# Performance work log

Measured on AMD Instinct MI355X. Metric: run time of the kernel, lower is better.

The kernel has to match this reference:

```python
import jax, jax.numpy as jnp
from jax import lax
import numpy as np

EPS = 1e-5


def _fps(xyz, S):
    B, N, _ = xyz.shape

    def step(carry, _):
        dist, far = carry  # [B,N], [B]
        c = xyz[jnp.arange(B), far]               # [B,3]
        d = jnp.sum((xyz - c[:, None, :]) ** 2, -1)  # [B,N]
        dist = jnp.minimum(dist, d)
        nxt = jnp.argmax(dist, -1).astype(jnp.int32)
        return (dist, nxt), far

    init = (jnp.full((B, N), 1e10, xyz.dtype), jnp.zeros((B,), jnp.int32))
    _, idxs = lax.scan(step, init, None, length=S)
    return jnp.transpose(idxs)  # [B,S]


def _gather(pts, idx):
    # pts: [B,N,C], idx: [B,...] -> [B,...,C]
    return jax.vmap(lambda p, i: p[i])(pts, idx)


def _conv(x, W, b):
    # 1x1 Conv1d: x [M,Cin,L], W [Cout,Cin], b [Cout]
    return jnp.einsum('mcl,oc->mol', x, W) + b[None, :, None]


def _bn(x, g, b):
    # BatchNorm1d (training-mode batch stats, biased variance)
    mu = jnp.mean(x, (0, 2), keepdims=True)
    v = jnp.var(x, (0, 2), keepdims=True)
    return g[None, :, None] * (x - mu) / jnp.sqrt(v + EPS) + b[None, :, None]


def _forward(xyz, feature, affine_alpha, affine_beta, w_tr, b_tr, g_tr, be_tr,
             w1, b1, g1, be1, w2, b2, groups, k):
    xyz = jnp.transpose(xyz, (0, 2, 1))        # [B,N,3]
    feature = jnp.transpose(feature, (0, 2, 1))  # [B,N,D]
    B, N, _ = xyz.shape
    S = groups
    xyz_ng = lax.stop_gradient(xyz)  # cluster() runs under torch.no_grad
    fps_idx = _fps(xyz_ng, S)                        # [B,S]
    new_xyz = _gather(xyz_ng, fps_idx)               # [B,S,3] (detached)
    # squared-distance kNN: [B,S,N]
    sqr = (jnp.sum(new_xyz ** 2, -1)[:, :, None]
           + jnp.sum(xyz_ng ** 2, -1)[:, None, :]
           - 2.0 * jnp.einsum('bsc,bnc->bsn', new_xyz, xyz_ng))
    _, idx = lax.top_k(-sqr, k)                      # [B,S,k] smallest distances
    new_feature = _gather(feature, fps_idx)          # [B,S,D]
    grouped_xyz = _gather(xyz, idx)                  # [B,S,k,3]
    grouped_feature = _gather(feature, idx)          # [B,S,k,D]
    grouped_feature = jnp.concatenate([grouped_feature, grouped_xyz], -1)  # [B,S,k,D+3]
    # anchor normalization
    mean = jnp.concatenate([new_feature, new_xyz], -1)[:, :, None, :]  # [B,S,1,D+3]
    diff = grouped_feature - mean
    std = jnp.std(diff.reshape(B, -1), axis=-1, ddof=1)[:, None, None, None]
    gf = affine_alpha * (diff / (std + EPS)) + affine_beta
    # concat anchor feature -> [B,S,k,2D+3]
    D = new_feature.shape[-1]
    x = jnp.concatenate([gf, jnp.broadcast_to(new_feature[:, :, None, :], (B, S, k, D))], -1)
    d = x.shape[-1]
    # PreExtraction: [B,S,k,d] -> [B*S,d,k]
    x = jnp.transpose(x, (0, 1, 3, 2)).reshape(B * S, d, k)
    x = jax.nn.relu(_bn(_conv(x, w_tr, b_tr), g_tr, be_tr))
    y = jax.nn.relu(_bn(_conv(x, w1, b1), g1, be1))
    y = _conv(y, w2, b2)
    x = jax.nn.relu(y + x)
    x = jnp.max(x, -1).reshape(B, S, -1)             # adaptive_max_pool1d(1)
    return (jnp.transpose(new_xyz, (0, 2, 1)), jnp.transpose(x, (0, 2, 1)))


def setup_inputs() -> dict:
    key = jax.random.key(0)
    k0, k1, k2, k3, k4 = jax.random.split(key, 5)
    B, N, D = 8, 4096, 64
    return {
        'xyz': jax.random.normal(k0, (B, 3, N), jnp.float32),
        'feature': jax.random.normal(k1, (B, D, N), jnp.float32),
        'affine_alpha': jnp.ones((1, 1, 1, D + 3), jnp.float32),
        'affine_beta': jnp.zeros((1, 1, 1, D + 3), jnp.float32),
        'w_tr': 0.05 * jax.random.normal(k2, (D, 3 + 2 * D), jnp.float32),
        'b_tr': jnp.zeros((D,), jnp.float32),
        'g_tr': jnp.ones((D,), jnp.float32),
        'be_tr': jnp.zeros((D,), jnp.float32),
        'w1': 0.05 * jax.random.normal(k3, (D, D), jnp.float32),
        'b1': jnp.zeros((D,), jnp.float32),
        'g1': jnp.ones((D,), jnp.float32),
        'be1': jnp.zeros((D,), jnp.float32),
        'w2': 0.05 * jax.random.normal(k4, (D, D), jnp.float32),
        'b2': jnp.zeros((D,), jnp.float32),
        'groups': 1024,
        'k': 32,
    }


def reference(xyz, feature, affine_alpha, affine_beta, w_tr, b_tr, g_tr, be_tr,
              w1, b1, g1, be1, w2, b2, groups, k):
    return _forward(xyz, feature, affine_alpha, affine_beta, w_tr, b_tr, g_tr, be_tr,
                    w1, b1, g1, be1, w2, b2, groups, k)
```

## Files before the change

### kernel.cpp

```cpp
#include <hip/hip_runtime.h>
#include <cfloat>
#include <math.h>

#define B_ 8
#define N_ 4096
#define D_ 64
#define S_ 1024
#define K_ 32
#define CIN_ 131

typedef float f32x2 __attribute__((ext_vector_type(2)));

template <int CTRL>
__device__ __forceinline__ unsigned long long dpp_u64(unsigned long long k) {
  int lo = (int)(unsigned int)k, hi = (int)(unsigned int)(k >> 32);
  lo = __builtin_amdgcn_update_dpp(lo, lo, CTRL, 0xf, 0xf, false);
  hi = __builtin_amdgcn_update_dpp(hi, hi, CTRL, 0xf, 0xf, false);
  return ((unsigned long long)(unsigned int)hi << 32) | (unsigned int)lo;
}

__device__ __forceinline__ float wave_max_f32_dpp(float v) {
  int x = __float_as_int(v);
#define STEP(ctrl)                                                        \
  {                                                                       \
    int t = __builtin_amdgcn_update_dpp(x, x, ctrl, 0xf, 0xf, false);     \
    v = fmaxf(v, __int_as_float(t));                                      \
    x = __float_as_int(v);                                                \
  }
  STEP(0x111)
  STEP(0x112)
  STEP(0x114)
  STEP(0x118)
  STEP(0x142)
  STEP(0x143)
#undef STEP
  return __int_as_float(__builtin_amdgcn_readlane(x, 63));
}

__global__ __launch_bounds__(256) void fps_kernel(const float* __restrict__ xyz,
                                                  int* __restrict__ fps_idx,
                                                  float* __restrict__ nxyz,
                                                  float* __restrict__ out0,
                                                  const float* __restrict__ feature,
                                                  float* __restrict__ featT) {
#pragma clang fp contract(off)
  const int tid = threadIdx.x;
  __shared__ __align__(16) float4 sp[N_];
  __shared__ int si[S_];
  __shared__ unsigned long long keyp[2][4];
  if (blockIdx.x >= 8) {
    const int blk = blockIdx.x - 8;
    const int b = blk >> 6, n0 = (blk & 63) * 64;
    float* tile = (float*)sp;
#pragma unroll
    for (int i = 0; i < 16; i++) {
      int c = i * 4 + (tid >> 6), nl = tid & 63;
      tile[c * 65 + nl] = feature[((size_t)b * 64 + c) * N_ + n0 + nl];
    }
    __syncthreads();
#pragma unroll
    for (int i = 0; i < 16; i++) {
      int nl = i * 4 + (tid >> 6), c = tid & 63;
      featT[((size_t)b * N_ + n0 + nl) * 64 + c] = tile[c * 65 + nl];
    }
    return;
  }
  const int b = blockIdx.x;
  const float* xb = xyz + (size_t)b * 3 * N_;
  const float4* xv = (const float4*)xb;
  f32x2 pxv[8], pyv[8], pzv[8];
  float dist[16];
#pragma unroll
  for (int q = 0; q < 4; q++) {
    float4 X = xv[4 * tid + q];
    float4 Y = xv[1024 + 4 * tid + q];
    float4 Z = xv[2048 + 4 * tid + q];
    pxv[2 * q] = (f32x2){X.x, X.y};  pxv[2 * q + 1] = (f32x2){X.z, X.w};
    pyv[2 * q] = (f32x2){Y.x, Y.y};  pyv[2 * q + 1] = (f32x2){Y.z, Y.w};
    pzv[2 * q] = (f32x2){Z.x, Z.y};  pzv[2 * q + 1] = (f32x2){Z.z, Z.w};
  }
#pragma unroll
  for (int j = 0; j < 8; j++) {
    dist[2 * j] = 1e10f;
    dist[2 * j + 1] = 1e10f;
    sp[16 * tid + 2 * j] = make_float4(pxv[j].x, pyv[j].x, pzv[j].x, 0.f);
    sp[16 * tid + 2 * j + 1] = make_float4(pxv[j].y, pyv[j].y, pzv[j].y, 0.f);
  }
  if (tid == 0) si[0] = 0;
  __syncthreads();
  float cx = sp[0].x, cy = sp[0].y, cz = sp[0].z;
  const int wav = tid >> 6, lane = tid & 63;
  for (int s = 1; s < S_; s++) {
    const f32x2 c2x = {cx, cx}, c2y = {cy, cy}, c2z = {cz, cz};
#pragma unroll
    for (int j = 0; j < 8; j++) {
      f32x2 dx = pxv[j] - c2x;
      f32x2 dy = pyv[j] - c2y;
      f32x2 dz = pzv[j] - c2z;
      f32x2 d = (dx * dx + dy * dy) + dz * dz;
      dist[2 * j] = fminf(dist[2 * j], d.x);
      dist[2 * j + 1] = fminf(dist[2 * j + 1], d.y);
    }
    float t8[8], t4[4];
#pragma unroll
    for (int j = 0; j < 8; j++) t8[j] = fmaxf(dist[2 * j], dist[2 * j + 1]);
#pragma unroll
    for (int j = 0; j < 4; j++) t4[j] = fmaxf(t8[2 * j], t8[2 * j + 1]);
    float best = fmaxf(fmaxf(t4[0], t4[1]), fmaxf(t4[2], t4[3]));
    int bi = 16 * tid;
#pragma unroll
    for (int i = 15; i >= 0; i--)
      if (dist[i] == best) bi = 16 * tid + i;
    float wmax = wave_max_f32_dpp(best);
    unsigned long long m = __ballot(best == wmax);
    int l = __ffsll(m) - 1;
    int widx = __builtin_amdgcn_readlane(bi, l);
    if (lane == 0)
      keyp[s & 1][wav] =
          ((unsigned long long)(unsigned int)__float_as_int(wmax) << 32) |
          (unsigned int)(4095 - widx);
    __syncthreads();
    unsigned long long k = keyp[s & 1][lane & 3];
    unsigned long long t;
    t = dpp_u64<0xB1>(k); if (t > k) k = t;
    t = dpp_u64<0x4E>(k); if (t > k) k = t;
    int bix = 4095 - (int)(k & 0xfffull);
    if (tid == 0) si[s] = bix;
    float4 c = sp[bix];
    cx = c.x; cy = c.y; cz = c.z;
  }
  __syncthreads();
  for (int e = tid; e < S_; e += 256) {
    int n = si[e];
    fps_idx[b * S_ + e] = n;
    float4 c = sp[n];
    nxyz[(size_t)(b * S_ + e) * 3 + 0] = c.x;
    nxyz[(size_t)(b * S_ + e) * 3 + 1] = c.y;
    nxyz[(size_t)(b * S_ + e) * 3 + 2] = c.z;
    out0[(size_t)b * 3 * S_ + e] = c.x;
    out0[(size_t)b * 3 * S_ + S_ + e] = c.y;
    out0[(size_t)b * 3 * S_ + 2 * S_ + e] = c.z;
  }
}

__global__ __launch_bounds__(256) void knn_kernel(const float* __restrict__ xyz,
                                                  const float* __restrict__ nxyz,
                                                  int* __restrict__ knn,
                                                  const float* __restrict__ featT,
                                                  const int* __restrict__ fps_i,
                                                  float* __restrict__ nfeat) {
#pragma clang fp contract(off)
  const int bs = blockIdx.x, tid = threadIdx.x;
  if (bs >= 8192) {
    int e = (bs - 8192) * 256 + tid;
    int bsx = e >> 6, c = e & 63;
    int bq = bsx >> 10;
    int n = fps_i[bsx];
    nfeat[e] = featT[((size_t)bq * N_ + n) * 64 + c];
    return;
  }
  const int b = bs >> 10;
  const float* xb = xyz + (size_t)b * 3 * N_;
  const float cx = nxyz[(size_t)bs * 3], cy = nxyz[(size_t)bs * 3 + 1], cz = nxyz[(size_t)bs * 3 + 2];
  const float cn = (cx * cx + cy * cy) + cz * cz;
  const f32x2 c2x = {cx, cx}, c2y = {cy, cy}, c2z = {cz, cz};
  const f32x2 c2n = {cn, cn}, two = {2.0f, 2.0f};
  float d[16];
#pragma unroll
  for (int j = 0; j < 8; j++) {
    int n0 = (2 * j) * 256 + tid, n1 = n0 + 256;
    f32x2 px = {xb[n0], xb[n1]};
    f32x2 py = {xb[N_ + n0], xb[N_ + n1]};
    f32x2 pz = {xb[2 * N_ + n0], xb[2 * N_ + n1]};
    f32x2 pn = (px * px + py * py) + pz * pz;
    f32x2 dot = (c2x * px + c2y * py) + c2z * pz;
    f32x2 dd = (c2n + pn) - two * dot;
    d[2 * j] = dd.x;
    d[2 * j + 1] = dd.y;
  }
  float mv = FLT_MAX;
  int mi = tid;
#pragma unroll
  for (int i = 0; i < 16; i++)
    if (d[i] < mv) { mv = d[i]; mi = i * 256 + tid; }
  __shared__ unsigned long long keyp[2][4];
  __shared__ int skk[K_];
  const int wav = tid >> 6, lane = tid & 63;
  for (int j = 0; j < K_; j++) {
    unsigned int u = __float_as_uint(mv);
    u ^= ((unsigned int)((int)u >> 31) | 0x80000000u);
    unsigned long long key = ((unsigned long long)u << 32) | (unsigned int)mi;
#pragma unroll
    for (int off = 32; off >= 1; off >>= 1) {
      unsigned long long ok = __shfl_xor(key, off);
      if (ok < key) key = ok;
    }
    if (lane == 0) keyp[j & 1][wav] = key;
    __syncthreads();
    unsigned long long kmin = keyp[j & 1][0];
#pragma unroll
    for (int w = 1; w < 4; w++) {
      unsigned long long k2 = keyp[j & 1][w];
      if (k2 < kmin) kmin = k2;
    }
    int g = (int)(kmin & 0xffffffffull);
    if (tid == 0) skk[j] = g;
    if ((g & 255) == tid) {
      int sl = g >> 8;
#pragma unroll
      for (int i = 0; i < 16; i++)
        if (i == sl) d[i] = FLT_MAX;
      mv = FLT_MAX; mi = tid;
#pragma unroll
      for (int i = 0; i < 16; i++)
        if (d[i] < mv) { mv = d[i]; mi = i * 256 + tid; }
    }
  }
  __syncthreads();
  if (tid < K_) knn[(size_t)bs * K_ + tid] = skk[tid];
}

__global__ __launch_bounds__(256) void gather_nf(const float* __restrict__ feature,
                                                 const int* __restrict__ fps_i,
                                                 float* __restrict__ nfeat) {
  int e = blockIdx.x * 256 + threadIdx.x;
  int b = e >> 16, rem = e & 65535;
  int s = rem >> 6, c = rem & 63;
  int n = fps_i[b * S_ + s];
  nfeat[e] = feature[((size_t)b * 64 + c) * N_ + n];
}

__global__ __launch_bounds__(256) void std_partial(const float* __restrict__ feature,
                                                   const float* __restrict__ xyz,
                                                   const float* __restrict__ nxyz,
                                                   const float* __restrict__ nfeat,
                                                   const int* __restrict__ knn,
                                                   float* __restrict__ outp) {
  const int blk = blockIdx.x, tid = threadIdx.x;
  const int b = blk >> 6, chunk = blk & 63;
  float s = 0.f, q = 0.f;
  for (int e = tid; e < 16 * K_ * 67; e += 256) {
    int so = e / (K_ * 67);
    int rem = e - so * (K_ * 67);
    int kk = rem / 67;
    int c = rem - kk * 67;
    int bs = b * S_ + chunk * 16 + so;
    int n = knn[(size_t)bs * K_ + kk];
    float raw = (c < 64) ? feature[((size_t)b * 64 + c) * N_ + n]
                         : xyz[((size_t)b * 3 + (c - 64)) * N_ + n];
    float anc = (c < 64) ? nfeat[(size_t)bs * 64 + c]
                         : nxyz[(size_t)bs * 3 + (c - 64)];
    float dd = raw - anc;
    s += dd; q += dd * dd;
  }
#pragma unroll
  for (int off = 32; off >= 1; off >>= 1) { s += __shfl_xor(s, off); q += __shfl_xor(q, off); }
  __shared__ float rs[4], rq[4];
  if ((tid & 63) == 0) { rs[tid >> 6] = s; rq[tid >> 6] = q; }
  __syncthreads();
  if (tid == 0) {
    outp[blk * 2] = rs[0] + rs[1] + rs[2] + rs[3];
    outp[blk * 2 + 1] = rq[0] + rq[1] + rq[2] + rq[3];
  }
}

__global__ void std_final(const float* __restrict__ part, float* __restrict__ invstd) {
  int b = threadIdx.x;
  if (b < B_) {
    double s = 0.0, q = 0.0;
    for (int i = 0; i < 64; i++) {
      s += (double)part[(b * 64 + i) * 2];
      q += (double)part[(b * 64 + i) * 2 + 1];
    }
    const double n = (double)(S_ * K_ * 67);
    double var = (q - s * s / n) / (n - 1.0);
    invstd[b] = (float)(1.0 / (sqrt(var) + 1e-5));
  }
}

template <int MODE>
__global__ __launch_bounds__(256, 2) void mlp_kernel(
    const float* __restrict__ feature, const float* __restrict__ xyz,
    const float* __restrict__ nxyz, const float* __restrict__ nfeat,
    const int* __restrict__ knn, const float* __restrict__ invstd,
    const float* __restrict__ alpha, const float* __restrict__ beta,
    const float* __restrict__ w_tr, const float* __restrict__ b_tr,
    const float* __restrict__ w1, const float* __restrict__ b1,
    const float* __restrict__ w2, const float* __restrict__ b2,
    const float* __restrict__ bn_tr, const float* __restrict__ bn_1,
    float* __restrict__ bnpart, float* __restrict__ out1) {
  __shared__ __align__(16) float pool[15556];
  float* Wt = pool;
  float* xin = pool + 8516;
  float* ub = xin;
  float* tb = pool + 8516 + 4192;
  float* part = pool + 8516 + 4192 + 2304;
  int* sknn = (int*)(part + 512);
  const int bs = blockIdx.x, tid = threadIdx.x;
  const int b = bs >> 10, s = bs & 1023;
  if (tid < K_) sknn[tid] = knn[(size_t)bs * K_ + tid];
  for (int e = tid; e < 64 * 131; e += 256) {
    int o = e / 131, c = e - o * 131;
    Wt[c * 65 + o] = w_tr[e];
  }
  __syncthreads();
  const float inv = invstd[b];
  for (int e = tid; e < CIN_ * K_; e += 256) {
    int c = e >> 5, kk = e & 31;
    float v;
    if (c < 67) {
      int n = sknn[kk];
      float raw = (c < 64) ? feature[((size_t)b * 64 + c) * N_ + n]
                           : xyz[((size_t)b * 3 + (c - 64)) * N_ + n];
      float anc = (c < 64) ? nfeat[(size_t)bs * 64 + c]
                           : nxyz[(size_t)bs * 3 + (c - 64)];
      v = alpha[c] * ((raw - anc) * inv) + beta[c];
    } else {
      v = nfeat[(size_t)bs * 64 + (c - 67)];
    }
    xin[e] = v;
  }
  __syncthreads();
  const int o = tid & 63, kkb = (tid >> 6) * 8;
  float acc[8];
  {
    float bv = b_tr[o];
#pragma unroll
    for (int j = 0; j < 8; j++) acc[j] = bv;
  }
  for (int c = 0; c < CIN_; c++) {
    float w = Wt[c * 65 + o];
    const float4 xa = *(const float4*)(xin + c * 32 + kkb);
    const float4 xb4 = *(const float4*)(xin + c * 32 + kkb + 4);
    acc[0] += w * xa.x; acc[1] += w * xa.y; acc[2] += w * xa.z; acc[3] += w * xa.w;
    acc[4] += w * xb4.x; acc[5] += w * xb4.y; acc[6] += w * xb4.z; acc[7] += w * xb4.w;
  }
  if (MODE == 0) {
    float s8 = 0.f, q8 = 0.f;
#pragma unroll
    for (int j = 0; j < 8; j++) { s8 += acc[j]; q8 += acc[j] * acc[j]; }
    part[(tid >> 6) * 64 + o] = s8;
    part[256 + (tid >> 6) * 64 + o] = q8;
    __syncthreads();
    if (tid < 64) {
      float ss = 0.f, qq = 0.f;
      for (int g = 0; g < 4; g++) { ss += part[g * 64 + tid]; qq += part[256 + g * 64 + tid]; }
      bnpart[(size_t)bs * 128 + tid] = ss;
      bnpart[(size_t)bs * 128 + 64 + tid] = qq;
    }
    return;
  }
  float tv[8];
  {
    float sc = bn_tr[o], sh = bn_tr[64 + o];
#pragma unroll
    for (int j = 0; j < 8; j++) {
      tv[j] = fmaxf(fmaf(sc, acc[j], sh), 0.f);
      tb[o * 36 + kkb + j] = tv[j];
    }
  }
  __syncthreads();
  for (int e = tid; e < 64 * 64; e += 256) {
    int oo = e >> 6, c = e & 63;
    Wt[c * 65 + oo] = w1[e];
  }
  __syncthreads();
  float acc2[8];
  {
    float bv = b1[o];
#pragma unroll
    for (int j = 0; j < 8; j++) acc2[j] = bv;
  }
  for (int c = 0; c < 64; c++) {
    float w = Wt[c * 65 + o];
    const float4 ta = *(const float4*)(tb + c * 36 + kkb);
    const float4 ta2 = *(const float4*)(tb + c * 36 + kkb + 4);
    acc2[0] += w * ta.x; acc2[1] += w * ta.y; acc2[2] += w * ta.z; acc2[3] += w * ta.w;
    acc2[4] += w * ta2.x; acc2[5] += w * ta2.y; acc2[6] += w * ta2.z; acc2[7] += w * ta2.w;
  }
  if (MODE == 1) {
    float s8 = 0.f, q8 = 0.f;
#pragma unroll
    for (int j = 0; j < 8; j++) { s8 += acc2[j]; q8 += acc2[j] * acc2[j]; }
    part[(tid >> 6) * 64 + o] = s8;
    part[256 + (tid >> 6) * 64 + o] = q8;
    __syncthreads();
    if (tid < 64) {
      float ss = 0.f, qq = 0.f;
      for (int g = 0; g < 4; g++) { ss += part[g * 64 + tid]; qq += part[256 + g * 64 + tid]; }
      bnpart[(size_t)bs * 128 + tid] = ss;
      bnpart[(size_t)bs * 128 + 64 + tid] = qq;
    }
    return;
  }
  {
    float sc = bn_1[o], sh = bn_1[64 + o];
#pragma unroll
    for (int j = 0; j < 8; j++) ub[o * 36 + kkb + j] = fmaxf(fmaf(sc, acc2[j], sh), 0.f);
  }
  __syncthreads();
  for (int e = tid; e < 64 * 64; e += 256) {
    int oo = e >> 6, c = e & 63;
    Wt[c * 65 + oo] = w2[e];
  }
  __syncthreads();
  float acc3[8];
  {
    float bv = b2[o];
#pragma unroll
    for (int j = 0; j < 8; j++) acc3[j] = bv;
  }
  for (int c = 0; c < 64; c++) {
    float w = Wt[c * 65 + o];
    const float4 ua = *(const float4*)(ub + c * 36 + kkb);
    const float4 ua2 = *(const float4*)(ub + c * 36 + kkb + 4);
    acc3[0] += w * ua.x; acc3[1] += w * ua.y; acc3[2] += w * ua.z; acc3[3] += w * ua.w;
    acc3[4] += w * ua2.x; acc3[5] += w * ua2.y; acc3[6] += w * ua2.z; acc3[7] += w * ua2.w;
  }
  float m = 0.f;
#pragma unroll
  for (int j = 0; j < 8; j++) m = fmaxf(m, fmaxf(acc3[j] + tv[j], 0.f));
  part[(tid >> 6) * 64 + o] = m;
  __syncthreads();
  if (tid < 64) {
    float mm = part[tid];
    for (int g = 1; g < 4; g++) mm = fmaxf(mm, part[g * 64 + tid]);
    out1[((size_t)b * 64 + tid) * S_ + s] = mm;
  }
}

__global__ __launch_bounds__(256) void bn_finalize(const float* __restrict__ part,
                                                   const float* __restrict__ g,
                                                   const float* __restrict__ be,
                                                   float* __restrict__ bnout) {
  const int ch = blockIdx.x, tid = threadIdx.x;
  double s = 0.0, q = 0.0;
  for (int i = tid; i < B_ * S_; i += 256) {
    s += (double)part[(size_t)i * 128 + ch];
    q += (double)part[(size_t)i * 128 + 64 + ch];
  }
#pragma unroll
  for (int off = 32; off >= 1; off >>= 1) { s += __shfl_xor(s, off); q += __shfl_xor(q, off); }
  __shared__ double ls[4], lq[4];
  if ((tid & 63) == 0) { ls[tid >> 6] = s; lq[tid >> 6] = q; }
  __syncthreads();
  if (tid == 0) {
    double Ssum = ls[0] + ls[1] + ls[2] + ls[3];
    double Qsum = lq[0] + lq[1] + lq[2] + lq[3];
    const double n = (double)(B_ * S_ * K_);
    double mu = Ssum / n;
    double var = Qsum / n - mu * mu;
    double sc = (double)g[ch] / sqrt(var + 1e-5);
    bnout[ch] = (float)sc;
    bnout[64 + ch] = (float)((double)be[ch] - mu * sc);
  }
}


__global__ __launch_bounds__(256) void prep_kernel(const float* __restrict__ featT,
                                                   const float* __restrict__ xyz,
                                                   const float* __restrict__ nxyz,
                                                   const float* __restrict__ nfeat,
                                                   const int* __restrict__ knn,
                                                   float* __restrict__ dcache,
                                                   float* __restrict__ outp) {
  const int blk = blockIdx.x, tid = threadIdx.x;
  __shared__ int sk[32];
  float s = 0.f, q = 0.f;
  const int c = tid & 63, qd = tid >> 6;
  for (int g = 0; g < 8; g++) {
    const int bs = blk * 8 + g, b = bs >> 10;
    if (tid < 32) sk[tid] = knn[(size_t)bs * K_ + tid];
    __syncthreads();
    float anc = nfeat[(size_t)bs * 64 + c];
#pragma unroll
    for (int it = 0; it < 8; it++) {
      int kk = it * 4 + qd;
      int n = sk[kk];
      float dd = featT[((size_t)b * N_ + n) * 64 + c] - anc;
      s += dd; q += dd * dd;
      dcache[((size_t)bs * 32 + kk) * 68 + c] = dd;
    }
    if (tid < 96) {
      int c3 = tid >> 5, kk = tid & 31;
      int n = sk[kk];
      float dd = xyz[((size_t)b * 3 + c3) * N_ + n] - nxyz[(size_t)bs * 3 + c3];
      s += dd; q += dd * dd;
      dcache[((size_t)bs * 32 + kk) * 68 + 64 + c3] = dd;
    }
    __syncthreads();
  }
#pragma unroll
  for (int off = 32; off >= 1; off >>= 1) { s += __shfl_xor(s, off); q += __shfl_xor(q, off); }
  __shared__ float rs[4], rq[4];
  if ((tid & 63) == 0) { rs[tid >> 6] = s; rq[tid >> 6] = q; }
  __syncthreads();
  if (tid == 0) {
    outp[blk * 2] = rs[0] + rs[1] + rs[2] + rs[3];
    outp[blk * 2 + 1] = rq[0] + rq[1] + rq[2] + rq[3];
  }
}

__global__ void std_final_c(const float* __restrict__ part, float* __restrict__ invstd) {
  int b = threadIdx.x;
  if (b < B_) {
    double s = 0.0, q = 0.0;
    for (int i = 0; i < 128; i++) {
      s += (double)part[(b * 128 + i) * 2];
      q += (double)part[(b * 128 + i) * 2 + 1];
    }
    const double n = (double)(S_ * K_ * 67);
    double var = (q - s * s / n) / (n - 1.0);
    invstd[b] = (float)(1.0 / (sqrt(var) + 1e-5));
  }
}

__global__ __launch_bounds__(256, 2) void mlp0c(
    const float* __restrict__ dcache, const float* __restrict__ nfeat,
    const float* __restrict__ invstd,
    const float* __restrict__ alpha, const float* __restrict__ beta,
    const float* __restrict__ w_tr, const float* __restrict__ b_tr,
    float* __restrict__ bnpart, float* __restrict__ tcache) {
  __shared__ __align__(16) float pool[13220];
  float* Wt = pool;
  float* xin = pool + 8516;
  float* part = pool + 8516 + 4192;
  const int bs = blockIdx.x, tid = threadIdx.x;
  const int b = bs >> 10;
  for (int e = tid; e < 64 * 131; e += 256) {
    int o = e / 131, c = e - o * 131;
    Wt[c * 65 + o] = w_tr[e];
  }
  const float inv = invstd[b];
  {
    const int c = tid & 63, qd = tid >> 6;
    float al = alpha[c], bev = beta[c];
#pragma unroll
    for (int it = 0; it < 8; it++) {
      int kk = it * 4 + qd;
      xin[c * 32 + kk] = al * (dcache[((size_t)bs * 32 + kk) * 68 + c] * inv) + bev;
    }
    if (tid < 96) {
      int c3 = 64 + (tid >> 5), kk = tid & 31;
      xin[c3 * 32 + kk] =
          alpha[c3] * (dcache[((size_t)bs * 32 + kk) * 68 + c3] * inv) + beta[c3];
    }
    for (int e = tid; e < 2048; e += 256) {
      int cc = 67 + (e >> 5), kk = e & 31;
      xin[cc * 32 + kk] = nfeat[(size_t)bs * 64 + (e >> 5)];
    }
  }
  __syncthreads();
  const int o = tid & 63, kkb = (tid >> 6) * 8;
  float acc[8];
  {
    float bv = b_tr[o];
#pragma unroll
    for (int j = 0; j < 8; j++) acc[j] = bv;
  }
  for (int c = 0; c < CIN_; c++) {
    float w = Wt[c * 65 + o];
    const float4 xa = *(const float4*)(xin + c * 32 + kkb);
    const float4 xb4 = *(const float4*)(xin + c * 32 + kkb + 4);
    acc[0] += w * xa.x; acc[1] += w * xa.y; acc[2] += w * xa.z; acc[3] += w * xa.w;
    acc[4] += w * xb4.x; acc[5] += w * xb4.y; acc[6] += w * xb4.z; acc[7] += w * xb4.w;
  }
  {
    float4* tp = (float4*)(tcache + ((size_t)bs * 64 + o) * 32 + kkb);
    tp[0] = make_float4(acc[0], acc[1], acc[2], acc[3]);
    tp[1] = make_float4(acc[4], acc[5], acc[6], acc[7]);
  }
  float s8 = 0.f, q8 = 0.f;
#pragma unroll
  for (int j = 0; j < 8; j++) { s8 += acc[j]; q8 += acc[j] * acc[j]; }
  part[(tid >> 6) * 64 + o] = s8;
  part[256 + (tid >> 6) * 64 + o] = q8;
  __syncthreads();
  if (tid < 64) {
    float ss = 0.f, qq = 0.f;
    for (int g = 0; g < 4; g++) { ss += part[g * 64 + tid]; qq += part[256 + g * 64 + tid]; }
    bnpart[(size_t)bs * 128 + tid] = ss;
    bnpart[(size_t)bs * 128 + 64 + tid] = qq;
  }
}

__global__ __launch_bounds__(256, 3) void mlp1c(
    const float* __restrict__ tcache, const float* __restrict__ bn_tr,
    const float* __restrict__ w1, const float* __restrict__ b1,
    float* __restrict__ bnpart, float* __restrict__ ucache) {
  __shared__ __align__(16) float pool[6976];
  float* Wt = pool;
  float* tb = pool + 4160;
  float* part = pool + 4160 + 2304;
  const int bs = blockIdx.x, tid = threadIdx.x;
  const int o = tid & 63, kkb = (tid >> 6) * 8;
  for (int e = tid; e < 64 * 64; e += 256) {
    int oo = e >> 6, c = e & 63;
    Wt[c * 65 + oo] = w1[e];
  }
  float t[8];
  {
    const float4* tp = (const float4*)(tcache + ((size_t)bs * 64 + o) * 32 + kkb);
    float4 a = tp[0], b4 = tp[1];
    t[0] = a.x; t[1] = a.y; t[2] = a.z; t[3] = a.w;
    t[4] = b4.x; t[5] = b4.y; t[6] = b4.z; t[7] = b4.w;
  }
  {
    float sc = bn_tr[o], sh = bn_tr[64 + o];
#pragma unroll
    for (int j = 0; j < 8; j++) tb[o * 36 + kkb + j] = fmaxf(fmaf(sc, t[j], sh), 0.f);
  }
  __syncthreads();
  float acc2[8];
  {
    float bv = b1[o];
#pragma unroll
    for (int j = 0; j < 8; j++) acc2[j] = bv;
  }
  for (int c = 0; c < 64; c++) {
    float w = Wt[c * 65 + o];
    const float4 ta = *(const float4*)(tb + c * 36 + kkb);
    const float4 ta2 = *(const float4*)(tb + c * 36 + kkb + 4);
    acc2[0] += w * ta.x; acc2[1] += w * ta.y; acc2[2] += w * ta.z; acc2[3] += w * ta.w;
    acc2[4] += w * ta2.x; acc2[5] += w * ta2.y; acc2[6] += w * ta2.z; acc2[7] += w * ta2.w;
  }
  {
    float4* up = (float4*)(ucache + ((size_t)bs * 64 + o) * 32 + kkb);
    up[0] = make_float4(acc2[0], acc2[1], acc2[2], acc2[3]);
    up[1] = make_float4(acc2[4], acc2[5], acc2[6], acc2[7]);
  }
  float s8 = 0.f, q8 = 0.f;
#pragma unroll
  for (int j = 0; j < 8; j++) { s8 += acc2[j]; q8 += acc2[j] * acc2[j]; }
  part[(tid >> 6) * 64 + o] = s8;
  part[256 + (tid >> 6) * 64 + o] = q8;
  __syncthreads();
  if (tid < 64) {
    float ss = 0.f, qq = 0.f;
    for (int g = 0; g < 4; g++) { ss += part[g * 64 + tid]; qq += part[256 + g * 64 + tid]; }
    bnpart[(size_t)bs * 128 + tid] = ss;
    bnpart[(size_t)bs * 128 + 64 + tid] = qq;
  }
}

__global__ __launch_bounds__(256, 3) void mlp2c(
    const float* __restrict__ tcache, const float* __restrict__ ucache,
    const float* __restrict__ bn_tr, const float* __restrict__ bn_1,
    const float* __restrict__ w2, const float* __restrict__ b2,
    float* __restrict__ out1) {
  __shared__ __align__(16) float pool[6976];
  float* Wt = pool;
  float* ub = pool + 4160;
  float* part = pool + 4160 + 2304;
  const int bs = blockIdx.x, tid = threadIdx.x;
  const int b = bs >> 10, s = bs & 1023;
  const int o = tid & 63, kkb = (tid >> 6) * 8;
  for (int e = tid; e < 64 * 64; e += 256) {
    int oo = e >> 6, c = e & 63;
    Wt[c * 65 + oo] = w2[e];
  }
  {
    const float4* up = (const float4*)(ucache + ((size_t)bs * 64 + o) * 32 + kkb);
    float4 a = up[0], b4 = up[1];
    float u[8] = {a.x, a.y, a.z, a.w, b4.x, b4.y, b4.z, b4.w};
    float sc = bn_1[o], sh = bn_1[64 + o];
#pragma unroll
    for (int j = 0; j < 8; j++) ub[o * 36 + kkb + j] = fmaxf(fmaf(sc, u[j], sh), 0.f);
  }
  __syncthreads();
  float acc3[8];
  {
    float bv = b2[o];
#pragma unroll
    for (int j = 0; j < 8; j++) acc3[j] = bv;
  }
  for (int c = 0; c < 64; c++) {
    float w = Wt[c * 65 + o];
    const float4 ua = *(const float4*)(ub + c * 36 + kkb);
    const float4 ua2 = *(const float4*)(ub + c * 36 + kkb + 4);
    acc3[0] += w * ua.x; acc3[1] += w * ua.y; acc3[2] += w * ua.z; acc3[3] += w * ua.w;
    acc3[4] += w * ua2.x; acc3[5] += w * ua2.y; acc3[6] += w * ua2.z; acc3[7] += w * ua2.w;
  }
  float tv[8];
  {
    const float4* tp = (const float4*)(tcache + ((size_t)bs * 64 + o) * 32 + kkb);
    float4 a = tp[0], b4 = tp[1];
    float t[8] = {a.x, a.y, a.z, a.w, b4.x, b4.y, b4.z, b4.w};
    float sc = bn_tr[o], sh = bn_tr[64 + o];
#pragma unroll
    for (int j = 0; j < 8; j++) tv[j] = fmaxf(fmaf(sc, t[j], sh), 0.f);
  }
  float m = 0.f;
#pragma unroll
  for (int j = 0; j < 8; j++) m = fmaxf(m, fmaxf(acc3[j] + tv[j], 0.f));
  part[(tid >> 6) * 64 + o] = m;
  __syncthreads();
  if (tid < 64) {
    float mm = part[tid];
    for (int g = 1; g < 4; g++) mm = fmaxf(mm, part[g * 64 + tid]);
    out1[((size_t)b * 64 + tid) * S_ + s] = mm;
  }
}

extern "C" void kernel_launch(void* const* d_in, const int* in_sizes, int n_in,
                              void* d_out, int out_size, void* d_ws, size_t ws_size,
                              hipStream_t stream) {
  const float* xyz = (const float*)d_in[0];
  const float* feature = (const float*)d_in[1];
  const float* alpha = (const float*)d_in[2];
  const float* beta = (const float*)d_in[3];
  const float* w_tr = (const float*)d_in[4];
  const float* b_tr = (const float*)d_in[5];
  const float* g_tr = (const float*)d_in[6];
  const float* be_tr = (const float*)d_in[7];
  const float* w1 = (const float*)d_in[8];
  const float* b1 = (const float*)d_in[9];
  const float* g1 = (const float*)d_in[10];
  const float* be1 = (const float*)d_in[11];
  const float* w2 = (const float*)d_in[12];
  const float* b2 = (const float*)d_in[13];

  char* ws = (char*)d_ws;
  int* fps_i = (int*)(ws);
  float* nxyz = (float*)(ws + 32768);
  float* nfeat = (float*)(ws + 131072);
  int* knn = (int*)(ws + 2228224);
  float* stdpart = (float*)(ws + 3276800);
  float* invstd = (float*)(ws + 3280896);
  float* bn_tr = (float*)(ws + 3280960);
  float* bn_1 = (float*)(ws + 3281472);
  float* bnpart = (float*)(ws + 3281984);
  float* featT = (float*)(ws + 7476288);
  float* dcache = (float*)(ws + 15864896);
  float* tcache = (float*)(ws + 87168064);
  float* ucache = (float*)(ws + 154276928);
  float* stdpart_c = (float*)(ws + 221385792);

  float* out0 = (float*)d_out;
  float* out1 = out0 + B_ * 3 * S_;

  const bool big = (ws_size >= 221393984ull);

  if (big) {
    fps_kernel<<<8 + 512, 256, 0, stream>>>(xyz, fps_i, nxyz, out0, feature, featT);
    knn_kernel<<<8192 + 2048, 256, 0, stream>>>(xyz, nxyz, knn, featT, fps_i, nfeat);
    prep_kernel<<<1024, 256, 0, stream>>>(featT, xyz, nxyz, nfeat, knn, dcache, stdpart_c);
    std_final_c<<<1, 64, 0, stream>>>(stdpart_c, invstd);
    mlp0c<<<B_ * S_, 256, 0, stream>>>(dcache, nfeat, invstd, alpha, beta, w_tr, b_tr,
                                       bnpart, tcache);
    bn_finalize<<<64, 256, 0, stream>>>(bnpart, g_tr, be_tr, bn_tr);
    mlp1c<<<B_ * S_, 256, 0, stream>>>(tcache, bn_tr, w1, b1, bnpart, ucache);
    bn_finalize<<<64, 256, 0, stream>>>(bnpart, g1, be1, bn_1);
    mlp2c<<<B_ * S_, 256, 0, stream>>>(tcache, ucache, bn_tr, bn_1, w2, b2, out1);
  } else {
    fps_kernel<<<8, 256, 0, stream>>>(xyz, fps_i, nxyz, out0, feature, featT);
    gather_nf<<<(B_ * S_ * D_) / 256, 256, 0, stream>>>(feature, fps_i, nfeat);
    knn_kernel<<<8192, 256, 0, stream>>>(xyz, nxyz, knn, nullptr, nullptr, nullptr);
    std_partial<<<B_ * 64, 256, 0, stream>>>(feature, xyz, nxyz, nfeat, knn, stdpart);
    std_final<<<1, 64, 0, stream>>>(stdpart, invstd);
    mlp_kernel<0><<<B_ * S_, 256, 0, stream>>>(feature, xyz, nxyz, nfeat, knn, invstd,
                                               alpha, beta, w_tr, b_tr, w1, b1, w2, b2,
                                               bn_tr, bn_1, bnpart, out1);
    bn_finalize<<<64, 256, 0, stream>>>(bnpart, g_tr, be_tr, bn_tr);
    mlp_kernel<1><<<B_ * S_, 256, 0, stream>>>(feature, xyz, nxyz, nfeat, knn, invstd,
                                               alpha, beta, w_tr, b_tr, w1, b1, w2, b2,
                                               bn_tr, bn_1, bnpart, out1);
    bn_finalize<<<64, 256, 0, stream>>>(bnpart, g1, be1, bn_1);
    mlp_kernel<2><<<B_ * S_, 256, 0, stream>>>(feature, xyz, nxyz, nfeat, knn, invstd,
                                               alpha, beta, w_tr, b_tr, w1, b1, w2, b2,
                                               bn_tr, bn_1, bnpart, out1);
  }
}
```

Baseline: 1.141 ms.

## Run FPS on a single wavefront to drop per-iteration block barriers

The farthest-point-sampling loop now runs in one 64-lane wave per batch, with each lane holding 64 points in registers as packed float2 vectors. The running min and max use packed elementwise builtins. This removes the per-step __syncthreads and the cross-wave LDS key exchange, so the argmax comes straight from the wave-level DPP reduction and ballot. The cost is four times more arithmetic per lane on each step and much higher register pressure; __launch_bounds__(256,1) is added so the compiler can give the kernel more VGPRs.

After: 2.092 ms. 83.4% more time.

```diff
diff --git a/kernel.cpp b/kernel.cpp
--- a/kernel.cpp
+++ b/kernel.cpp
@@ -37,17 +37,16 @@
   return __int_as_float(__builtin_amdgcn_readlane(x, 63));
 }
 
-__global__ __launch_bounds__(256) void fps_kernel(const float* __restrict__ xyz,
-                                                  int* __restrict__ fps_idx,
-                                                  float* __restrict__ nxyz,
-                                                  float* __restrict__ out0,
-                                                  const float* __restrict__ feature,
-                                                  float* __restrict__ featT) {
+__global__ __launch_bounds__(256, 1) void fps_kernel(const float* __restrict__ xyz,
+                                                     int* __restrict__ fps_idx,
+                                                     float* __restrict__ nxyz,
+                                                     float* __restrict__ out0,
+                                                     const float* __restrict__ feature,
+                                                     float* __restrict__ featT) {
 #pragma clang fp contract(off)
   const int tid = threadIdx.x;
   __shared__ __align__(16) float4 sp[N_];
   __shared__ int si[S_];
-  __shared__ unsigned long long keyp[2][4];
   if (blockIdx.x >= 8) {
     const int blk = blockIdx.x - 8;
     const int b = blk >> 6, n0 = (blk & 63) * 64;
@@ -65,72 +64,66 @@
     }
     return;
   }
+  if (tid >= 64) return;
   const int b = blockIdx.x;
   const float* xb = xyz + (size_t)b * 3 * N_;
   const float4* xv = (const float4*)xb;
-  f32x2 pxv[8], pyv[8], pzv[8];
-  float dist[16];
-#pragma unroll
-  for (int q = 0; q < 4; q++) {
-    float4 X = xv[4 * tid + q];
-    float4 Y = xv[1024 + 4 * tid + q];
-    float4 Z = xv[2048 + 4 * tid + q];
-    pxv[2 * q] = (f32x2){X.x, X.y};  pxv[2 * q + 1] = (f32x2){X.z, X.w};
-    pyv[2 * q] = (f32x2){Y.x, Y.y};  pyv[2 * q + 1] = (f32x2){Y.z, Y.w};
-    pzv[2 * q] = (f32x2){Z.x, Z.y};  pzv[2 * q + 1] = (f32x2){Z.z, Z.w};
-  }
-#pragma unroll
-  for (int j = 0; j < 8; j++) {
-    dist[2 * j] = 1e10f;
-    dist[2 * j + 1] = 1e10f;
-    sp[16 * tid + 2 * j] = make_float4(pxv[j].x, pyv[j].x, pzv[j].x, 0.f);
-    sp[16 * tid + 2 * j + 1] = make_float4(pxv[j].y, pyv[j].y, pzv[j].y, 0.f);
-  }
+  f32x2 px[32], py[32], pz[32], dd[32];
+#pragma unroll
+  for (int q = 0; q < 16; q++) {
+    float4 X = xv[16 * tid + q];
+    float4 Y = xv[1024 + 16 * tid + q];
+    float4 Z = xv[2048 + 16 * tid + q];
+    px[2 * q] = (f32x2){X.x, X.y};  px[2 * q + 1] = (f32x2){X.z, X.w};
+    py[2 * q] = (f32x2){Y.x, Y.y};  py[2 * q + 1] = (f32x2){Y.z, Y.w};
+    pz[2 * q] = (f32x2){Z.x, Z.y};  pz[2 * q + 1] = (f32x2){Z.z, Z.w};
+    sp[64 * tid + 4 * q + 0] = make_float4(X.x, Y.x, Z.x, 0.f);
+    sp[64 * tid + 4 * q + 1] = make_float4(X.y, Y.y, Z.y, 0.f);
+    sp[64 * tid + 4 * q + 2] = make_float4(X.z, Y.z, Z.z, 0.f);
+    sp[64 * tid + 4 * q + 3] = make_float4(X.w, Y.w, Z.w, 0.f);
+  }
+#pragma unroll
+  for (int j = 0; j < 32; j++) dd[j] = (f32x2){1e10f, 1e10f};
   if (tid == 0) si[0] = 0;
-  __syncthreads();
-  float cx = sp[0].x, cy = sp[0].y, cz = sp[0].z;
-  const int wav = tid >> 6, lane = tid & 63;
+  float cx = __int_as_float(__builtin_amdgcn_readlane(__float_as_int(px[0].x), 0));
+  float cy = __int_as_float(__builtin_amdgcn_readlane(__float_as_int(py[0].x), 0));
+  float cz = __int_as_float(__builtin_amdgcn_readlane(__float_as_int(pz[0].x), 0));
   for (int s = 1; s < S_; s++) {
     const f32x2 c2x = {cx, cx}, c2y = {cy, cy}, c2z = {cz, cz};
 #pragma unroll
-    for (int j = 0; j < 8; j++) {
-      f32x2 dx = pxv[j] - c2x;
-      f32x2 dy = pyv[j] - c2y;
-      f32x2 dz = pzv[j] - c2z;
+    for (int j = 0; j < 32; j++) {
+      f32x2 dx = px[j] - c2x;
+      f32x2 dy = py[j] - c2y;
+      f32x2 dz = pz[j] - c2z;
       f32x2 d = (dx * dx + dy * dy) + dz * dz;
-      dist[2 * j] = fminf(dist[2 * j], d.x);
-      dist[2 * j + 1] = fminf(dist[2 * j + 1], d.y);
-    }
-    float t8[8], t4[4];
-#pragma unroll
-    for (int j = 0; j < 8; j++) t8[j] = fmaxf(dist[2 * j], dist[2 * j + 1]);
-#pragma unroll
-    for (int j = 0; j < 4; j++) t4[j] = fmaxf(t8[2 * j], t8[2 * j + 1]);
-    float best = fmaxf(fmaxf(t4[0], t4[1]), fmaxf(t4[2], t4[3]));
-    int bi = 16 * tid;
-#pragma unroll
-    for (int i = 15; i >= 0; i--)
-      if (dist[i] == best) bi = 16 * tid + i;
+      dd[j] = __builtin_elementwise_min(dd[j], d);
+    }
+    f32x2 m16[16], m8[8], m4[4], m2[2];
+#pragma unroll
+    for (int j = 0; j < 16; j++) m16[j] = __builtin_elementwise_max(dd[2 * j], dd[2 * j + 1]);
+#pragma unroll
+    for (int j = 0; j < 8; j++) m8[j] = __builtin_elementwise_max(m16[2 * j], m16[2 * j + 1]);
+#pragma unroll
+    for (int j = 0; j < 4; j++) m4[j] = __builtin_elementwise_max(m8[2 * j], m8[2 * j + 1]);
+#pragma unroll
+    for (int j = 0; j < 2; j++) m2[j] = __builtin_elementwise_max(m4[2 * j], m4[2 * j + 1]);
+    f32x2 m1 = __builtin_elementwise_max(m2[0], m2[1]);
+    float best = fmaxf(m1.x, m1.y);
+    int bi = 64 * tid;
+#pragma unroll
+    for (int j = 31; j >= 0; j--) {
+      if (dd[j].y == best) bi = 64 * tid + 2 * j + 1;
+      if (dd[j].x == best) bi = 64 * tid + 2 * j;
+    }
     float wmax = wave_max_f32_dpp(best);
-    unsigned long long m = __ballot(best == wmax);
-    int l = __ffsll(m) - 1;
+    unsigned long long mm = __ballot(best == wmax);
+    int l = __ffsll(mm) - 1;
     int widx = __builtin_amdgcn_readlane(bi, l);
-    if (lane == 0)
-      keyp[s & 1][wav] =
-          ((unsigned long long)(unsigned int)__float_as_int(wmax) << 32) |
-          (unsigned int)(4095 - widx);
-    __syncthreads();
-    unsigned long long k = keyp[s & 1][lane & 3];
-    unsigned long long t;
-    t = dpp_u64<0xB1>(k); if (t > k) k = t;
-    t = dpp_u64<0x4E>(k); if (t > k) k = t;
-    int bix = 4095 - (int)(k & 0xfffull);
-    if (tid == 0) si[s] = bix;
-    float4 c = sp[bix];
+    if (tid == 0) si[s] = widx;
+    float4 c = sp[widx];
     cx = c.x; cy = c.y; cz = c.z;
   }
-  __syncthreads();
-  for (int e = tid; e < S_; e += 256) {
+  for (int e = tid; e < S_; e += 64) {
     int n = si[e];
     fps_idx[b * S_ + e] = n;
     float4 c = sp[n];
```

## Fuse FPS and kNN into one persistent kernel with flag-based streaming

Applied to the files above, without the earlier changes.

Replaces the separate FPS and kNN launches with one persistent kernel. Eight blocks run FPS and publish progress flags every 32 samples, while the other 504 blocks first transpose features, then run kNN on centroids as soon as they are published. The aim is to hide kNN work behind the long serial FPS loop. The cost is that correctness depends on all 512 blocks being co-resident for the spin-waits, and it adds global atomics and a memset.

Measured after the change: 1.601 ms. 40.4% more time.

```diff
diff --git a/kernel.cpp b/kernel.cpp
--- a/kernel.cpp
+++ b/kernel.cpp
@@ -35,6 +35,195 @@
   STEP(0x143)
 #undef STEP
   return __int_as_float(__builtin_amdgcn_readlane(x, 63));
+}
+
+__global__ __launch_bounds__(256) void fps_knn_fused(
+    const float* __restrict__ xyz, int* __restrict__ fps_idx,
+    float* __restrict__ nxyz, float* __restrict__ out0,
+    const float* __restrict__ feature, float* __restrict__ featT,
+    unsigned int* __restrict__ flags,
+    int* __restrict__ knn_out, float* __restrict__ nfeat) {
+#pragma clang fp contract(off)
+  const int tid = threadIdx.x;
+  __shared__ __align__(16) float4 sp[N_];
+  __shared__ int si[S_];
+  __shared__ unsigned long long keyp[2][4];
+  if (blockIdx.x >= 8) {
+    const int bid = blockIdx.x - 8;
+    float* tile = (float*)sp;
+    for (int t = bid; t < 512; t += 504) {
+      const int tb = t >> 6, n0 = (t & 63) * 64;
+#pragma unroll
+      for (int i = 0; i < 16; i++) {
+        int c = i * 4 + (tid >> 6), nl = tid & 63;
+        tile[c * 65 + nl] = feature[((size_t)tb * 64 + c) * N_ + n0 + nl];
+      }
+      __syncthreads();
+#pragma unroll
+      for (int i = 0; i < 16; i++) {
+        int nl = i * 4 + (tid >> 6), c = tid & 63;
+        featT[((size_t)tb * N_ + n0 + nl) * 64 + c] = tile[c * 65 + nl];
+      }
+      __syncthreads();
+    }
+    if (tid == 0)
+      __hip_atomic_fetch_add(&flags[8], 1u, __ATOMIC_RELEASE, __HIP_MEMORY_SCOPE_AGENT);
+    while (__hip_atomic_load(&flags[8], __ATOMIC_ACQUIRE, __HIP_MEMORY_SCOPE_AGENT) < 504u)
+      __builtin_amdgcn_s_sleep(8);
+    __syncthreads();
+
+    int* skk = si;
+    const int wav = tid >> 6, lane = tid & 63;
+    for (int p = bid; p < 8192; p += 504) {
+      const int b = p >> 10, s = p & 1023, bs = p;
+      const unsigned int need = (unsigned int)(s >> 5) + 1u;
+      while (__hip_atomic_load(&flags[b], __ATOMIC_ACQUIRE, __HIP_MEMORY_SCOPE_AGENT) < need)
+        __builtin_amdgcn_s_sleep(8);
+      const float* xb = xyz + (size_t)b * 3 * N_;
+      const float cx = nxyz[(size_t)bs * 3], cy = nxyz[(size_t)bs * 3 + 1],
+                  cz = nxyz[(size_t)bs * 3 + 2];
+      const float cn = (cx * cx + cy * cy) + cz * cz;
+      const f32x2 c2x = {cx, cx}, c2y = {cy, cy}, c2z = {cz, cz};
+      const f32x2 c2n = {cn, cn}, two = {2.0f, 2.0f};
+      float d[16];
+#pragma unroll
+      for (int j = 0; j < 8; j++) {
+        int n0 = (2 * j) * 256 + tid, n1 = n0 + 256;
+        f32x2 px = {xb[n0], xb[n1]};
+        f32x2 py = {xb[N_ + n0], xb[N_ + n1]};
+        f32x2 pz = {xb[2 * N_ + n0], xb[2 * N_ + n1]};
+        f32x2 pn = (px * px + py * py) + pz * pz;
+        f32x2 dot = (c2x * px + c2y * py) + c2z * pz;
+        f32x2 dd = (c2n + pn) - two * dot;
+        d[2 * j] = dd.x;
+        d[2 * j + 1] = dd.y;
+      }
+      float mv = FLT_MAX;
+      int mi = tid;
+#pragma unroll
+      for (int i = 0; i < 16; i++)
+        if (d[i] < mv) { mv = d[i]; mi = i * 256 + tid; }
+      for (int j = 0; j < K_; j++) {
+        unsigned int u = __float_as_uint(mv);
+        u ^= ((unsigned int)((int)u >> 31) | 0x80000000u);
+        unsigned long long key = ((unsigned long long)u << 32) | (unsigned int)mi;
+#pragma unroll
+        for (int off = 32; off >= 1; off >>= 1) {
+          unsigned long long ok = __shfl_xor(key, off);
+          if (ok < key) key = ok;
+        }
+        if (lane == 0) keyp[j & 1][wav] = key;
+        __syncthreads();
+        unsigned long long kmin = keyp[j & 1][0];
+#pragma unroll
+        for (int w = 1; w < 4; w++) {
+          unsigned long long k2 = keyp[j & 1][w];
+          if (k2 < kmin) kmin = k2;
+        }
+        int g = (int)(kmin & 0xffffffffull);
+        if (tid == 0) skk[j] = g;
+        if ((g & 255) == tid) {
+          int sl = g >> 8;
+#pragma unroll
+          for (int i = 0; i < 16; i++)
+            if (i == sl) d[i] = FLT_MAX;
+          mv = FLT_MAX; mi = tid;
+#pragma unroll
+          for (int i = 0; i < 16; i++)
+            if (d[i] < mv) { mv = d[i]; mi = i * 256 + tid; }
+        }
+      }
+      __syncthreads();
+      if (tid < K_) knn_out[(size_t)bs * K_ + tid] = skk[tid];
+      if (tid < 64) {
+        int nc = fps_idx[bs];
+        nfeat[(size_t)bs * 64 + tid] = featT[((size_t)b * N_ + nc) * 64 + tid];
+      }
+      __syncthreads();
+    }
+    return;
+  }
+  const int b = blockIdx.x;
+  const float* xb = xyz + (size_t)b * 3 * N_;
+  const float4* xv = (const float4*)xb;
+  f32x2 pxv[8], pyv[8], pzv[8];
+  float dist[16];
+#pragma unroll
+  for (int q = 0; q < 4; q++) {
+    float4 X = xv[4 * tid + q];
+    float4 Y = xv[1024 + 4 * tid + q];
+    float4 Z = xv[2048 + 4 * tid + q];
+    pxv[2 * q] = (f32x2){X.x, X.y};  pxv[2 * q + 1] = (f32x2){X.z, X.w};
+    pyv[2 * q] = (f32x2){Y.x, Y.y};  pyv[2 * q + 1] = (f32x2){Y.z, Y.w};
+    pzv[2 * q] = (f32x2){Z.x, Z.y};  pzv[2 * q + 1] = (f32x2){Z.z, Z.w};
+  }
+#pragma unroll
+  for (int j = 0; j < 8; j++) {
+    dist[2 * j] = 1e10f;
+    dist[2 * j + 1] = 1e10f;
+    sp[16 * tid + 2 * j] = make_float4(pxv[j].x, pyv[j].x, pzv[j].x, 0.f);
+    sp[16 * tid + 2 * j + 1] = make_float4(pxv[j].y, pyv[j].y, pzv[j].y, 0.f);
+  }
+  if (tid == 0) si[0] = 0;
+  __syncthreads();
+  float cx = sp[0].x, cy = sp[0].y, cz = sp[0].z;
+  const int wav = tid >> 6, lane = tid & 63;
+  for (int s = 1; s < S_; s++) {
+    const f32x2 c2x = {cx, cx}, c2y = {cy, cy}, c2z = {cz, cz};
+#pragma unroll
+    for (int j = 0; j < 8; j++) {
+      f32x2 dx = pxv[j] - c2x;
+      f32x2 dy = pyv[j] - c2y;
+      f32x2 dz = pzv[j] - c2z;
+      f32x2 d = (dx * dx + dy * dy) + dz * dz;
+      dist[2 * j] = fminf(dist[2 * j], d.x);
+      dist[2 * j + 1] = fminf(dist[2 * j + 1], d.y);
+    }
+    float t8[8], t4[4];
+#pragma unroll
+    for (int j = 0; j < 8; j++) t8[j] = fmaxf(dist[2 * j], dist[2 * j + 1]);
+#pragma unroll
+    for (int j = 0; j < 4; j++) t4[j] = fmaxf(t8[2 * j], t8[2 * j + 1]);
+    float best = fmaxf(fmaxf(t4[0], t4[1]), fmaxf(t4[2], t4[3]));
+    int bi = 16 * tid;
+#pragma unroll
+    for (int i = 15; i >= 0; i--)
+      if (dist[i] == best) bi = 16 * tid + i;
+    float wmax = wave_max_f32_dpp(best);
+    unsigned long long m = __ballot(best == wmax);
+    int l = __ffsll(m) - 1;
+    int widx = __builtin_amdgcn_readlane(bi, l);
+    if (lane == 0)
+      keyp[s & 1][wav] =
+          ((unsigned long long)(unsigned int)__float_as_int(wmax) << 32) |
+          (unsigned int)(4095 - widx);
+    __syncthreads();
+    unsigned long long k = keyp[s & 1][lane & 3];
+    unsigned long long t;
+    t = dpp_u64<0xB1>(k); if (t > k) k = t;
+    t = dpp_u64<0x4E>(k); if (t > k) k = t;
+    int bix = 4095 - (int)(k & 0xfffull);
+    if (tid == 0) si[s] = bix;
+    float4 c = sp[bix];
+    cx = c.x; cy = c.y; cz = c.z;
+    if ((s & 31) == 31) {
+      if (tid < 32) {
+        int e = (s & ~31) + tid;
+        int n = si[e];
+        fps_idx[b * S_ + e] = n;
+        float4 cc = sp[n];
+        nxyz[(size_t)(b * S_ + e) * 3 + 0] = cc.x;
+        nxyz[(size_t)(b * S_ + e) * 3 + 1] = cc.y;
+        nxyz[(size_t)(b * S_ + e) * 3 + 2] = cc.z;
+        out0[(size_t)b * 3 * S_ + e] = cc.x;
+        out0[(size_t)b * 3 * S_ + S_ + e] = cc.y;
+        out0[(size_t)b * 3 * S_ + 2 * S_ + e] = cc.z;
+      }
+      if (tid == 0)
+        __hip_atomic_store(&flags[b], (unsigned int)((s >> 5) + 1),
+                           __ATOMIC_RELEASE, __HIP_MEMORY_SCOPE_AGENT);
+    }
+  }
 }
 
 __global__ __launch_bounds__(256) void fps_kernel(const float* __restrict__ xyz,
@@ -742,8 +931,10 @@
   const bool big = (ws_size >= 221393984ull);
 
   if (big) {
-    fps_kernel<<<8 + 512, 256, 0, stream>>>(xyz, fps_i, nxyz, out0, feature, featT);
-    knn_kernel<<<8192 + 2048, 256, 0, stream>>>(xyz, nxyz, knn, featT, fps_i, nfeat);
+    unsigned int* flags = (unsigned int*)(ws + 3276800);
+    hipMemsetAsync(flags, 0, 64, stream);
+    fps_knn_fused<<<512, 256, 0, stream>>>(xyz, fps_i, nxyz, out0, feature, featT,
+                                           flags, knn, nfeat);
     prep_kernel<<<1024, 256, 0, stream>>>(featT, xyz, nxyz, nfeat, knn, dcache, stdpart_c);
     std_final_c<<<1, 64, 0, stream>>>(stdpart_c, invstd);
     mlp0c<<<B_ * S_, 256, 0, stream>>>(dcache, nfeat, invstd, alpha, beta, w_tr, b_tr,
```
